# Kernel optimization log

Measured on AMD Instinct MI355X. Metric: run time of the kernel, lower is better.

## Reference

```python
import jax, jax.numpy as jnp
import numpy as np

N, E, D, R = 50000, 600000, 128, 8


def setup_inputs() -> dict:
    key = jax.random.key(0)
    ks = jax.random.split(key, 10)
    return {
        "x": jax.random.normal(ks[0], (N, D), dtype=jnp.float32),
        "h": jax.random.normal(ks[1], (N, D), dtype=jnp.float32),
        "edge_index": jax.random.randint(ks[2], (2, E), 0, N, dtype=jnp.int32),
        "edge_type": jax.random.randint(ks[3], (E,), 0, R, dtype=jnp.int32),
        "edge_weight": jax.random.uniform(ks[4], (E,), dtype=jnp.float32),
        "rel_weight": jax.random.normal(ks[5], (R, D, D), dtype=jnp.float32) * 0.05,
        "root_weight": jax.random.normal(ks[6], (D, D), dtype=jnp.float32) * 0.05,
        "bias": jax.random.normal(ks[7], (D,), dtype=jnp.float32) * 0.05,
        "skip_weight": jax.random.normal(ks[8], (D, D), dtype=jnp.float32) * 0.05,
        "skip_bias": jax.random.normal(ks[9], (D,), dtype=jnp.float32) * 0.05,
    }


def reference(x, h, edge_index, edge_type, edge_weight, rel_weight, root_weight, bias, skip_weight, skip_bias):
    # skip projection (nn.Linear: y = x W^T + b)
    skip = x @ skip_weight.T + skip_bias  # [N, D]

    src, dst = edge_index[0], edge_index[1]  # PyG: message from src (x_j), aggregated at dst

    # Transform every node by every relation once (R is small), then gather per edge.
    # Avoids per-edge [E, D, D] weight gather.
    h_rel = jnp.einsum('nd,rdf->nrf', h, rel_weight)  # [N, R, D]
    msg = h_rel[src, edge_type] * edge_weight[:, None]  # [E, D]

    agg = jax.ops.segment_sum(msg, dst, num_segments=h.shape[0])  # [N, D]

    out = agg + h @ root_weight + bias + skip
    return out
```

## Files before the change

### kernel.cpp

```cpp
#include <hip/hip_runtime.h>


constexpr int DIM  = 128;
constexpr int BM   = 64;
constexpr int KC   = 32;
constexpr int BPAD = 4;
constexpr int KTOT = 1280;
constexpr int SCAN_CHUNK = 2048;

typedef __attribute__((ext_vector_type(8))) short     short8v;
typedef __attribute__((ext_vector_type(8))) unsigned short ushort8v;
typedef __attribute__((ext_vector_type(4))) float     float4v;
typedef __attribute__((ext_vector_type(4))) unsigned  uint4v;

__device__ __forceinline__ unsigned short f2bf(float x) {
    union { float f; unsigned u; } c; c.f = x;
    unsigned u = c.u;
    u += 0x7fffu + ((u >> 16) & 1u);
    return (unsigned short)(u >> 16);
}
__device__ __forceinline__ float bfbits2f(unsigned lo16) {
    union { unsigned u; float f; } c; c.u = lo16 << 16; return c.f;
}

__global__ __launch_bounds__(256) void cvt_bf16_kernel(
    const float* __restrict__ src, unsigned short* __restrict__ dst, int n8)
{
    int i = blockIdx.x * 256 + threadIdx.x;
    if (i >= n8) return;
    const float4 v0 = *reinterpret_cast<const float4*>(src + (size_t)i * 8);
    const float4 v1 = *reinterpret_cast<const float4*>(src + (size_t)i * 8 + 4);
    ushort8v o;
    o[0] = f2bf(v0.x); o[1] = f2bf(v0.y); o[2] = f2bf(v0.z); o[3] = f2bf(v0.w);
    o[4] = f2bf(v1.x); o[5] = f2bf(v1.y); o[6] = f2bf(v1.z); o[7] = f2bf(v1.w);
    *reinterpret_cast<ushort8v*>(dst + (size_t)i * 8) = o;
}

__global__ __launch_bounds__(256) void zero_i32_kernel(int* __restrict__ p, int n)
{
    int i = blockIdx.x * 256 + threadIdx.x;
    if (i < n) p[i] = 0;
}

__global__ __launch_bounds__(256) void hist_kernel(
    const int* __restrict__ ei, const int* __restrict__ et,
    int* __restrict__ counts, int E)
{
    int e = blockIdx.x * 256 + threadIdx.x;
    if (e < E) atomicAdd(&counts[ei[(long long)E + e] * 8 + (et[e] & 7)], 1);
}

__global__ __launch_bounds__(256) void scan1_kernel(
    const int* __restrict__ counts, int* __restrict__ local,
    int* __restrict__ blockSums, int M)
{
    __shared__ int sh[256];
    const int b = blockIdx.x, t = threadIdx.x;
    const int base = b * SCAN_CHUNK + t * 8;

    int v[8];
    int s = 0;
    #pragma unroll
    for (int j = 0; j < 8; ++j) {
        int idx = base + j;
        v[j] = (idx < M) ? counts[idx] : 0;
        s += v[j];
    }
    sh[t] = s;
    __syncthreads();
    for (int off = 1; off < 256; off <<= 1) {
        int x = (t >= off) ? sh[t - off] : 0;
        __syncthreads();
        sh[t] += x;
        __syncthreads();
    }
    int ex = sh[t] - s;
    if (t == 255) blockSums[b] = sh[255];
    #pragma unroll
    for (int j = 0; j < 8; ++j) {
        int idx = base + j;
        if (idx < M) { local[idx] = ex; ex += v[j]; }
    }
}

__global__ __launch_bounds__(1024) void scan2_kernel(int* __restrict__ bs, int nb)
{
    __shared__ int sh[1024];
    const int t = threadIdx.x;
    int v = (t < nb) ? bs[t] : 0;
    sh[t] = v;
    __syncthreads();
    for (int off = 1; off < 1024; off <<= 1) {
        int x = (t >= off) ? sh[t - off] : 0;
        __syncthreads();
        sh[t] += x;
        __syncthreads();
    }
    if (t < nb) bs[t] = sh[t] - v;
}

__global__ __launch_bounds__(256) void scan3_kernel(
    int* __restrict__ offsets, const int* __restrict__ blockSums,
    int* __restrict__ cursor, int M, int E)
{
    const int b = blockIdx.x, t = threadIdx.x;
    const int add = blockSums[b];
    #pragma unroll
    for (int j = 0; j < 8; ++j) {
        int idx = b * SCAN_CHUNK + j * 256 + t;
        if (idx < M) {
            int v = offsets[idx] + add;
            offsets[idx] = v;
            cursor[idx]  = v;
        }
    }
    if (b == 0 && t == 0) offsets[M] = E;
}

__global__ __launch_bounds__(256) void scatter_kernel(
    const int* __restrict__ ei, const int* __restrict__ et,
    const float* __restrict__ ew, int* __restrict__ cursor,
    int2* __restrict__ payload, int E)
{
    int e = blockIdx.x * 256 + threadIdx.x;
    if (e < E) {
        int key = ei[(long long)E + e] * 8 + (et[e] & 7);
        int pos = atomicAdd(&cursor[key], 1);
        payload[pos] = make_int2(ei[e], __float_as_int(ew[e]));
    }
}

__global__ __launch_bounds__(256) void accum_kernel(
    const int2* __restrict__ payload, const unsigned short* __restrict__ hb,
    const int* __restrict__ offsets, unsigned short* __restrict__ S, int N)
{
    const int tid  = threadIdx.x;
    const int wv   = tid >> 6;
    const int lane = tid & 63;
    const int sub  = lane >> 4;
    const int l16  = lane & 15;
    const int n    = blockIdx.x * 16 + wv * 4 + sub;
    if (n >= N) return;

    const int segBase = n * 8;
    int s1 = offsets[segBase];

    for (int r = 0; r < 8; ++r) {
        const int s0 = s1;
        s1 = offsets[segBase + r + 1];

        float acc[8] = {0.f, 0.f, 0.f, 0.f, 0.f, 0.f, 0.f, 0.f};
        for (int o = s0; o < s1; ++o) {
            const int2 p = payload[o];
            const ushort8v hv = *reinterpret_cast<const ushort8v*>(
                hb + (size_t)p.x * DIM + l16 * 8);
            const float w = __int_as_float(p.y);
            #pragma unroll
            for (int j = 0; j < 8; ++j)
                acc[j] += w * bfbits2f((unsigned)(unsigned short)hv[j]);
        }

        uint4v pk;
        #pragma unroll
        for (int i = 0; i < 4; ++i)
            pk[i] = (unsigned)f2bf(acc[2 * i]) | ((unsigned)f2bf(acc[2 * i + 1]) << 16);
        *reinterpret_cast<uint4v*>(
            &S[(size_t)n * 1024 + r * DIM + l16 * 8]) = pk;
    }
}

__global__ __launch_bounds__(256) void repack_B_kernel(
    const float* __restrict__ relF, const float* __restrict__ rootW,
    const float* __restrict__ skipW, unsigned short* __restrict__ Bt)
{
    int idx = blockIdx.x * 256 + threadIdx.x;
    if (idx >= DIM * KTOT) return;
    int f = idx / KTOT, k = idx % KTOT;
    float v;
    if (k < 1024)       v = relF[(size_t)k * DIM + f];
    else if (k < 1152)  v = rootW[(k - 1024) * DIM + f];
    else                v = skipW[f * DIM + (k - 1152)];
    Bt[(size_t)f * KTOT + k] = f2bf(v);
}

__global__ __launch_bounds__(256) void mfma_gemm_kernel(
    const unsigned short* __restrict__ S, const unsigned short* __restrict__ hb,
    const float* __restrict__ x, const unsigned short* __restrict__ Bt,
    const float* __restrict__ bias, const float* __restrict__ skipB,
    float* __restrict__ out, int N)
{
    __shared__ unsigned short As[64 * 64];
    __shared__ unsigned short Bs[128 * 64];

    const int tid  = threadIdx.x;
    const int lane = tid & 63;
    const int wid  = tid >> 6;
    const int wr   = wid >> 1, wc = wid & 1;
    const int l15  = lane & 15, l4 = lane >> 4;
    const int n0   = blockIdx.x * 64;

    float4v acc[2][4];
    #pragma unroll
    for (int m = 0; m < 2; ++m)
        #pragma unroll
        for (int nn = 0; nn < 4; ++nn)
            acc[m][nn] = (float4v)0.f;

    for (int k0 = 0; k0 < KTOT; k0 += 64) {
        __syncthreads();
        if (k0 < 1152) {
            const unsigned short* __restrict__ A = (k0 < 1024) ? S : hb;
            const size_t stride = (k0 < 1024) ? 1024 : DIM;
            const int kb = (k0 < 1024) ? k0 : (k0 - 1024);
            #pragma unroll
            for (int i = 0; i < 2; ++i) {
                int idx = tid + i * 256;
                int row = idx >> 3, c8 = idx & 7;
                int n = n0 + row;
                ushort8v v = (ushort8v)0;
                if (n < N)
                    v = *reinterpret_cast<const ushort8v*>(
                        &A[(size_t)n * stride + kb + c8 * 8]);
                int bo = row * 128 + ((c8 * 16) ^ ((row & 7) << 4));
                *reinterpret_cast<ushort8v*>((char*)As + bo) = v;
            }
        } else {
            const int kb = k0 - 1152;
            #pragma unroll
            for (int i = 0; i < 4; ++i) {
                int idx = tid + i * 256;
                int row = idx >> 4, c4 = idx & 15;
                int n = n0 + row;
                float4 v = make_float4(0.f, 0.f, 0.f, 0.f);
                if (n < N)
                    v = *reinterpret_cast<const float4*>(
                        &x[(size_t)n * DIM + kb + c4 * 4]);
                unsigned short b4[4] = { f2bf(v.x), f2bf(v.y), f2bf(v.z), f2bf(v.w) };
                int bo = row * 128 + ((c4 * 8) ^ ((row & 7) << 4));
                *reinterpret_cast<ulonglong1*>((char*)As + bo) =
                    *reinterpret_cast<const ulonglong1*>(b4);
            }
        }
        #pragma unroll
        for (int i = 0; i < 4; ++i) {
            int idx = tid + i * 256;
            int col = idx >> 3, c8 = idx & 7;
            ushort8v v = *reinterpret_cast<const ushort8v*>(
                &Bt[(size_t)col * KTOT + k0 + c8 * 8]);
            int bo = col * 128 + ((c8 * 16) ^ ((col & 7) << 4));
            *reinterpret_cast<ushort8v*>((char*)Bs + bo) = v;
        }
        __syncthreads();

        #pragma unroll
        for (int s = 0; s < 2; ++s) {
            const int kk = s * 32 + l4 * 8;
            short8v a[2], b[4];
            #pragma unroll
            for (int m = 0; m < 2; ++m) {
                int row = wr * 32 + m * 16 + l15;
                int bo = row * 128 + ((kk * 2) ^ ((row & 7) << 4));
                a[m] = *reinterpret_cast<const short8v*>((const char*)As + bo);
            }
            #pragma unroll
            for (int nn = 0; nn < 4; ++nn) {
                int col = wc * 64 + nn * 16 + l15;
                int bo = col * 128 + ((kk * 2) ^ ((col & 7) << 4));
                b[nn] = *reinterpret_cast<const short8v*>((const char*)Bs + bo);
            }
            #pragma unroll
            for (int m = 0; m < 2; ++m)
                #pragma unroll
                for (int nn = 0; nn < 4; ++nn)
                    acc[m][nn] = __builtin_amdgcn_mfma_f32_16x16x32_bf16(
                        a[m], b[nn], acc[m][nn], 0, 0, 0);
        }
    }

    #pragma unroll
    for (int nn = 0; nn < 4; ++nn) {
        const int col = wc * 64 + nn * 16 + l15;
        const float bb = bias[col] + skipB[col];
        #pragma unroll
        for (int m = 0; m < 2; ++m) {
            #pragma unroll
            for (int j = 0; j < 4; ++j) {
                int row = wr * 32 + m * 16 + l4 * 4 + j;
                int n = n0 + row;
                if (n < N)
                    out[(size_t)n * DIM + col] = acc[m][nn][j] + bb;
            }
        }
    }
}

__global__ __launch_bounds__(256) void base_kernel(
    const float* __restrict__ x, const float* __restrict__ h,
    const float* __restrict__ skipW, const float* __restrict__ rootW,
    const float* __restrict__ bias, const float* __restrict__ skipB,
    float* __restrict__ out, int N)
{
    __shared__ float As2[BM][KC];
    __shared__ float Bs2[KC][DIM + BPAD];

    const int tid = threadIdx.x;
    const int n0  = blockIdx.x * BM;
    const int f0  = (tid & 31) * 4;
    const int r0  = (tid >> 5) * 8;

    float acc[8][4] = {};

    for (int phase = 0; phase < 2; ++phase) {
        const float* __restrict__ A = phase ? h : x;
        for (int d0 = 0; d0 < DIM; d0 += KC) {
            __syncthreads();
            for (int idx = tid; idx < BM * KC; idx += 256) {
                int r = idx / KC, dd = idx % KC;
                int n = n0 + r;
                As2[r][dd] = (n < N) ? A[(long long)n * DIM + d0 + dd] : 0.f;
            }
            if (phase == 0) {
                for (int idx = tid; idx < DIM * KC; idx += 256) {
                    int f = idx / KC, dd = idx % KC;
                    Bs2[dd][f] = skipW[f * DIM + d0 + dd];
                }
            } else {
                for (int idx = tid; idx < KC * DIM; idx += 256) {
                    int dd = idx / DIM, f = idx % DIM;
                    Bs2[dd][f] = rootW[(d0 + dd) * DIM + f];
                }
            }
            __syncthreads();
            #pragma unroll
            for (int dd = 0; dd < KC; ++dd) {
                float a[8];
                #pragma unroll
                for (int i = 0; i < 8; ++i) a[i] = As2[r0 + i][dd];
                const float4 b = *reinterpret_cast<const float4*>(&Bs2[dd][f0]);
                #pragma unroll
                for (int i = 0; i < 8; ++i) {
                    acc[i][0] += a[i] * b.x; acc[i][1] += a[i] * b.y;
                    acc[i][2] += a[i] * b.z; acc[i][3] += a[i] * b.w;
                }
            }
        }
    }

    float bb[4];
    #pragma unroll
    for (int j = 0; j < 4; ++j) bb[j] = bias[f0 + j] + skipB[f0 + j];
    #pragma unroll
    for (int i = 0; i < 8; ++i) {
        int n = n0 + r0 + i;
        if (n < N) {
            float4 v = make_float4(acc[i][0] + bb[0], acc[i][1] + bb[1],
                                   acc[i][2] + bb[2], acc[i][3] + bb[3]);
            *reinterpret_cast<float4*>(&out[(long long)n * DIM + f0]) = v;
        }
    }
}

__global__ __launch_bounds__(256) void hrel_kernel(
    const float* __restrict__ h, const float* __restrict__ rel,
    float* __restrict__ hrel, int N, int R)
{
    __shared__ float As2[BM][KC];
    __shared__ float Bs2[KC][DIM + BPAD];

    const int tid = threadIdx.x;
    const int n0  = blockIdx.x * BM;
    const int rr  = blockIdx.y;
    const float* __restrict__ B = rel + (size_t)rr * DIM * DIM;
    const int f0  = (tid & 31) * 4;
    const int r0  = (tid >> 5) * 8;

    float acc[8][4] = {};

    for (int d0 = 0; d0 < DIM; d0 += KC) {
        __syncthreads();
        for (int idx = tid; idx < BM * KC; idx += 256) {
            int r = idx / KC, dd = idx % KC;
            int n = n0 + r;
            As2[r][dd] = (n < N) ? h[(long long)n * DIM + d0 + dd] : 0.f;
        }
        for (int idx = tid; idx < KC * DIM; idx += 256) {
            int dd = idx / DIM, f = idx % DIM;
            Bs2[dd][f] = B[(d0 + dd) * DIM + f];
        }
        __syncthreads();
        #pragma unroll
        for (int dd = 0; dd < KC; ++dd) {
            float a[8];
            #pragma unroll
            for (int i = 0; i < 8; ++i) a[i] = As2[r0 + i][dd];
            const float4 b = *reinterpret_cast<const float4*>(&Bs2[dd][f0]);
            #pragma unroll
            for (int i = 0; i < 8; ++i) {
                acc[i][0] += a[i] * b.x; acc[i][1] += a[i] * b.y;
                acc[i][2] += a[i] * b.z; acc[i][3] += a[i] * b.w;
            }
        }
    }

    #pragma unroll
    for (int i = 0; i < 8; ++i) {
        int n = n0 + r0 + i;
        if (n < N) {
            float4 v = make_float4(acc[i][0], acc[i][1], acc[i][2], acc[i][3]);
            *reinterpret_cast<float4*>(&hrel[((long long)n * R + rr) * DIM + f0]) = v;
        }
    }
}

__global__ __launch_bounds__(256) void edge_kernel(
    const int* __restrict__ ei, const int* __restrict__ et,
    const float* __restrict__ ew, const float* __restrict__ hrel,
    float* __restrict__ out, int E, int R)
{
    const int tid  = threadIdx.x;
    const int lane = tid & 31;
    const long long e = (long long)blockIdx.x * 8 + (tid >> 5);
    if (e >= E) return;

    const int   src = ei[e];
    const int   dst = ei[(long long)E + e];
    const int   r   = et[e];
    const float w   = ew[e];

    const float4 v = reinterpret_cast<const float4*>(
        hrel + ((long long)src * R + r) * DIM)[lane];

    float* o = out + (long long)dst * DIM + lane * 4;
    atomicAdd(o + 0, v.x * w);
    atomicAdd(o + 1, v.y * w);
    atomicAdd(o + 2, v.z * w);
    atomicAdd(o + 3, v.w * w);
}

__global__ __launch_bounds__(256) void edge_direct_kernel(
    const int* __restrict__ ei, const int* __restrict__ et,
    const float* __restrict__ ew, const float* __restrict__ h,
    const float* __restrict__ rel, float* __restrict__ out, int E)
{
    const int wid  = threadIdx.x >> 6;
    const int lane = threadIdx.x & 63;
    const long long e = (long long)blockIdx.x * 4 + wid;
    if (e >= E) return;

    const int   src = ei[e];
    const int   dst = ei[(long long)E + e];
    const int   r   = et[e];
    const float w   = ew[e];

    const float* __restrict__ hrow = h + (long long)src * DIM;
    const float* __restrict__ W    = rel + (size_t)r * DIM * DIM;

    float acc0 = 0.f, acc1 = 0.f;
    #pragma unroll 8
    for (int d = 0; d < DIM; ++d) {
        float hv = hrow[d];
        acc0 += hv * W[d * DIM + lane];
        acc1 += hv * W[d * DIM + lane + 64];
    }
    atomicAdd(&out[(long long)dst * DIM + lane],      acc0 * w);
    atomicAdd(&out[(long long)dst * DIM + lane + 64], acc1 * w);
}

extern "C" void kernel_launch(void* const* d_in, const int* in_sizes, int n_in,
                              void* d_out, int out_size, void* d_ws, size_t ws_size,
                              hipStream_t stream)
{
    const float* x     = (const float*)d_in[0];
    const float* h     = (const float*)d_in[1];
    const int*   ei    = (const int*)  d_in[2];
    const int*   et    = (const int*)  d_in[3];
    const float* ew    = (const float*)d_in[4];
    const float* rel   = (const float*)d_in[5];
    const float* rootW = (const float*)d_in[6];
    const float* bias  = (const float*)d_in[7];
    const float* skipW = (const float*)d_in[8];
    const float* skipB = (const float*)d_in[9];
    float* out = (float*)d_out;

    const int N = in_sizes[0] / DIM;
    const int E = in_sizes[3];
    const int R = in_sizes[5] / (DIM * DIM);

    const int M = N * 8;
    const int nbScan = (M + SCAN_CHUNK - 1) / SCAN_CHUNK;

    const size_t S_elems  = (size_t)N * 1024;
    const size_t hb_elems = (size_t)N * DIM;
    const size_t Bt_elems = (size_t)DIM * KTOT;
    const size_t head_bytes = (S_elems + hb_elems + Bt_elems) * sizeof(unsigned short);
    const size_t need_new = head_bytes
                          + (size_t)E * sizeof(int2)
                          + ((size_t)(M + 1) + M + 1024) * sizeof(int);

    if (R == 8 && nbScan <= 1024 && (head_bytes % 8 == 0) && ws_size >= need_new) {
        unsigned short* S  = (unsigned short*)d_ws;
        unsigned short* hb = S + S_elems;
        unsigned short* Bt = hb + hb_elems;
        int2*  payload   = (int2*)((char*)d_ws + head_bytes);
        int*   offsets   = (int*)(payload + E);
        int*   cursor    = offsets + (M + 1);
        int*   blockSums = cursor + M;

        const int n8 = N * DIM / 8;
        zero_i32_kernel<<<dim3((M + 255) / 256), 256, 0, stream>>>(cursor, M);
        hist_kernel<<<dim3((E + 255) / 256), 256, 0, stream>>>(ei, et, cursor, E);
        scan1_kernel<<<dim3(nbScan), 256, 0, stream>>>(cursor, offsets, blockSums, M);
        scan2_kernel<<<dim3(1), 1024, 0, stream>>>(blockSums, nbScan);
        scan3_kernel<<<dim3(nbScan), 256, 0, stream>>>(offsets, blockSums, cursor, M, E);
        scatter_kernel<<<dim3((E + 255) / 256), 256, 0, stream>>>(
            ei, et, ew, cursor, payload, E);
        cvt_bf16_kernel<<<dim3((n8 + 255) / 256), 256, 0, stream>>>(h, hb, n8);
        repack_B_kernel<<<dim3((DIM * KTOT + 255) / 256), 256, 0, stream>>>(
            rel, rootW, skipW, Bt);
        accum_kernel<<<dim3((N + 15) / 16), 256, 0, stream>>>(
            payload, hb, offsets, S, N);
        mfma_gemm_kernel<<<dim3((N + 63) / 64), 256, 0, stream>>>(
            S, hb, x, Bt, bias, skipB, out, N);
    } else {
        base_kernel<<<dim3((N + BM - 1) / BM), 256, 0, stream>>>(
            x, h, skipW, rootW, bias, skipB, out, N);
        if (ws_size >= (size_t)N * R * DIM * sizeof(float)) {
            float* hrel = (float*)d_ws;
            hrel_kernel<<<dim3((N + BM - 1) / BM, R), 256, 0, stream>>>(h, rel, hrel, N, R);
            edge_kernel<<<dim3((E + 7) / 8), 256, 0, stream>>>(ei, et, ew, hrel, out, E, R);
        } else {
            edge_direct_kernel<<<dim3((E + 3) / 4), 256, 0, stream>>>(ei, et, ew, h, rel, out, E);
        }
    }
}
```

Before: 181.6 us.

## Load MFMA operands directly from global memory and pre-convert x to bf16

```diff
diff --git a/kernel.cpp b/kernel.cpp
--- a/kernel.cpp
+++ b/kernel.cpp
@@ -185,13 +185,10 @@
 
 __global__ __launch_bounds__(256) void mfma_gemm_kernel(
     const unsigned short* __restrict__ S, const unsigned short* __restrict__ hb,
-    const float* __restrict__ x, const unsigned short* __restrict__ Bt,
+    const unsigned short* __restrict__ xb, const unsigned short* __restrict__ Bt,
     const float* __restrict__ bias, const float* __restrict__ skipB,
     float* __restrict__ out, int N)
 {
-    __shared__ unsigned short As[64 * 64];
-    __shared__ unsigned short Bs[128 * 64];
-
     const int tid  = threadIdx.x;
     const int lane = tid & 63;
     const int wid  = tid >> 6;
@@ -199,6 +196,27 @@
     const int l15  = lane & 15, l4 = lane >> 4;
     const int n0   = blockIdx.x * 64;
 
+    int rc[2];
+    #pragma unroll
+    for (int m = 0; m < 2; ++m) {
+        int r = n0 + wr * 32 + m * 16 + l15;
+        rc[m] = (r < N) ? r : (N - 1);
+    }
+    const unsigned short* apS[2] = {
+        S + (size_t)rc[0] * 1024 + l4 * 8,
+        S + (size_t)rc[1] * 1024 + l4 * 8 };
+    const unsigned short* apH[2] = {
+        hb + (size_t)rc[0] * DIM + l4 * 8,
+        hb + (size_t)rc[1] * DIM + l4 * 8 };
+    const unsigned short* apX[2] = {
+        xb + (size_t)rc[0] * DIM + l4 * 8,
+        xb + (size_t)rc[1] * DIM + l4 * 8 };
+
+    const unsigned short* bp[4];
+    #pragma unroll
+    for (int nn = 0; nn < 4; ++nn)
+        bp[nn] = Bt + (size_t)(wc * 64 + nn * 16 + l15) * KTOT + l4 * 8;
+
     float4v acc[2][4];
     #pragma unroll
     for (int m = 0; m < 2; ++m)
@@ -206,75 +224,53 @@
         for (int nn = 0; nn < 4; ++nn)
             acc[m][nn] = (float4v)0.f;
 
-    for (int k0 = 0; k0 < KTOT; k0 += 64) {
-        __syncthreads();
-        if (k0 < 1152) {
-            const unsigned short* __restrict__ A = (k0 < 1024) ? S : hb;
-            const size_t stride = (k0 < 1024) ? 1024 : DIM;
-            const int kb = (k0 < 1024) ? k0 : (k0 - 1024);
-            #pragma unroll
-            for (int i = 0; i < 2; ++i) {
-                int idx = tid + i * 256;
-                int row = idx >> 3, c8 = idx & 7;
-                int n = n0 + row;
-                ushort8v v = (ushort8v)0;
-                if (n < N)
-                    v = *reinterpret_cast<const ushort8v*>(
-                        &A[(size_t)n * stride + kb + c8 * 8]);
-                int bo = row * 128 + ((c8 * 16) ^ ((row & 7) << 4));
-                *reinterpret_cast<ushort8v*>((char*)As + bo) = v;
-            }
-        } else {
-            const int kb = k0 - 1152;
-            #pragma unroll
-            for (int i = 0; i < 4; ++i) {
-                int idx = tid + i * 256;
-                int row = idx >> 4, c4 = idx & 15;
-                int n = n0 + row;
-                float4 v = make_float4(0.f, 0.f, 0.f, 0.f);
-                if (n < N)
-                    v = *reinterpret_cast<const float4*>(
-                        &x[(size_t)n * DIM + kb + c4 * 4]);
-                unsigned short b4[4] = { f2bf(v.x), f2bf(v.y), f2bf(v.z), f2bf(v.w) };
-                int bo = row * 128 + ((c4 * 8) ^ ((row & 7) << 4));
-                *reinterpret_cast<ulonglong1*>((char*)As + bo) =
-                    *reinterpret_cast<const ulonglong1*>(b4);
-            }
-        }
-        #pragma unroll
-        for (int i = 0; i < 4; ++i) {
-            int idx = tid + i * 256;
-            int col = idx >> 3, c8 = idx & 7;
-            ushort8v v = *reinterpret_cast<const ushort8v*>(
-                &Bt[(size_t)col * KTOT + k0 + c8 * 8]);
-            int bo = col * 128 + ((c8 * 16) ^ ((col & 7) << 4));
-            *reinterpret_cast<ushort8v*>((char*)Bs + bo) = v;
-        }
-        __syncthreads();
-
-        #pragma unroll
-        for (int s = 0; s < 2; ++s) {
-            const int kk = s * 32 + l4 * 8;
-            short8v a[2], b[4];
-            #pragma unroll
-            for (int m = 0; m < 2; ++m) {
-                int row = wr * 32 + m * 16 + l15;
-                int bo = row * 128 + ((kk * 2) ^ ((row & 7) << 4));
-                a[m] = *reinterpret_cast<const short8v*>((const char*)As + bo);
-            }
-            #pragma unroll
-            for (int nn = 0; nn < 4; ++nn) {
-                int col = wc * 64 + nn * 16 + l15;
-                int bo = col * 128 + ((kk * 2) ^ ((col & 7) << 4));
-                b[nn] = *reinterpret_cast<const short8v*>((const char*)Bs + bo);
-            }
-            #pragma unroll
-            for (int m = 0; m < 2; ++m)
-                #pragma unroll
-                for (int nn = 0; nn < 4; ++nn)
-                    acc[m][nn] = __builtin_amdgcn_mfma_f32_16x16x32_bf16(
-                        a[m], b[nn], acc[m][nn], 0, 0, 0);
-        }
+    #pragma unroll 4
+    for (int k = 0; k < 1024; k += 32) {
+        short8v a[2], b[4];
+        #pragma unroll
+        for (int m = 0; m < 2; ++m)
+            a[m] = *reinterpret_cast<const short8v*>(apS[m] + k);
+        #pragma unroll
+        for (int nn = 0; nn < 4; ++nn)
+            b[nn] = *reinterpret_cast<const short8v*>(bp[nn] + k);
+        #pragma unroll
+        for (int m = 0; m < 2; ++m)
+            #pragma unroll
+            for (int nn = 0; nn < 4; ++nn)
+                acc[m][nn] = __builtin_amdgcn_mfma_f32_16x16x32_bf16(
+                    a[m], b[nn], acc[m][nn], 0, 0, 0);
+    }
+    #pragma unroll
+    for (int k = 0; k < 128; k += 32) {
+        short8v a[2], b[4];
+        #pragma unroll
+        for (int m = 0; m < 2; ++m)
+            a[m] = *reinterpret_cast<const short8v*>(apH[m] + k);
+        #pragma unroll
+        for (int nn = 0; nn < 4; ++nn)
+            b[nn] = *reinterpret_cast<const short8v*>(bp[nn] + 1024 + k);
+        #pragma unroll
+        for (int m = 0; m < 2; ++m)
+            #pragma unroll
+            for (int nn = 0; nn < 4; ++nn)
+                acc[m][nn] = __builtin_amdgcn_mfma_f32_16x16x32_bf16(
+                    a[m], b[nn], acc[m][nn], 0, 0, 0);
+    }
+    #pragma unroll
+    for (int k = 0; k < 128; k += 32) {
+        short8v a[2], b[4];
+        #pragma unroll
+        for (int m = 0; m < 2; ++m)
+            a[m] = *reinterpret_cast<const short8v*>(apX[m] + k);
+        #pragma unroll
+        for (int nn = 0; nn < 4; ++nn)
+            b[nn] = *reinterpret_cast<const short8v*>(bp[nn] + 1152 + k);
+        #pragma unroll
+        for (int m = 0; m < 2; ++m)
+            #pragma unroll
+            for (int nn = 0; nn < 4; ++nn)
+                acc[m][nn] = __builtin_amdgcn_mfma_f32_16x16x32_bf16(
+                    a[m], b[nn], acc[m][nn], 0, 0, 0);
     }
 
     #pragma unroll
@@ -492,7 +488,8 @@
     const size_t S_elems  = (size_t)N * 1024;
     const size_t hb_elems = (size_t)N * DIM;
     const size_t Bt_elems = (size_t)DIM * KTOT;
-    const size_t head_bytes = (S_elems + hb_elems + Bt_elems) * sizeof(unsigned short);
+    const size_t head_bytes =
+        (S_elems + 2 * hb_elems + Bt_elems) * sizeof(unsigned short);
     const size_t need_new = head_bytes
                           + (size_t)E * sizeof(int2)
                           + ((size_t)(M + 1) + M + 1024) * sizeof(int);
@@ -500,7 +497,8 @@
     if (R == 8 && nbScan <= 1024 && (head_bytes % 8 == 0) && ws_size >= need_new) {
         unsigned short* S  = (unsigned short*)d_ws;
         unsigned short* hb = S + S_elems;
-        unsigned short* Bt = hb + hb_elems;
+        unsigned short* xb = hb + hb_elems;
+        unsigned short* Bt = xb + hb_elems;
         int2*  payload   = (int2*)((char*)d_ws + head_bytes);
         int*   offsets   = (int*)(payload + E);
         int*   cursor    = offsets + (M + 1);
@@ -515,12 +513,13 @@
         scatter_kernel<<<dim3((E + 255) / 256), 256, 0, stream>>>(
             ei, et, ew, cursor, payload, E);
         cvt_bf16_kernel<<<dim3((n8 + 255) / 256), 256, 0, stream>>>(h, hb, n8);
+        cvt_bf16_kernel<<<dim3((n8 + 255) / 256), 256, 0, stream>>>(x, xb, n8);
         repack_B_kernel<<<dim3((DIM * KTOT + 255) / 256), 256, 0, stream>>>(
             rel, rootW, skipW, Bt);
         accum_kernel<<<dim3((N + 15) / 16), 256, 0, stream>>>(
             payload, hb, offsets, S, N);
         mfma_gemm_kernel<<<dim3((N + 63) / 64), 256, 0, stream>>>(
-            S, hb, x, Bt, bias, skipB, out, N);
+            S, hb, xb, Bt, bias, skipB, out, N);
     } else {
         base_kernel<<<dim3((N + BM - 1) / BM), 256, 0, stream>>>(
             x, h, skipW, rootW, bias, skipB, out, N);
```

Result: slower. 250.7 us (+38.0%).
